# Kernel tuning notes

Measured on AMD Instinct MI355X. Metric: run time of the kernel, lower is better.

## Reference

```python
import jax, jax.numpy as jnp
import numpy as np

N = 20000       # nodes
E = 320000      # edges (before self-loops)
F_IN = 1024     # num_features
H = 4           # head_num
C = 64          # hidden_size
NC = 4          # n_classes
NEG_SLOPE = 0.2 # PyG GATConv default


def setup_inputs() -> dict:
    key = jax.random.key(0)
    ks = jax.random.split(key, 16)
    def w(k, shape, fan_in):
        return jax.random.normal(k, shape, dtype=jnp.float32) / np.sqrt(fan_in)
    x = jax.random.normal(ks[0], (N, F_IN), dtype=jnp.float32)
    edge_index = jax.random.randint(ks[1], (2, E), 0, N, dtype=jnp.int64)
    return {
        "x": x,
        "edge_index": edge_index,
        # layer 1: F_IN -> H*C, concat
        "w1": w(ks[2], (F_IN, H * C), F_IN),
        "as1": w(ks[3], (H, C), C),
        "ad1": w(ks[4], (H, C), C),
        "b1": jnp.zeros((H * C,), jnp.float32),
        # layer 2: H*C -> H*C, concat
        "w2": w(ks[5], (H * C, H * C), H * C),
        "as2": w(ks[6], (H, C), C),
        "ad2": w(ks[7], (H, C), C),
        "b2": jnp.zeros((H * C,), jnp.float32),
        # out layer: H*C -> C, 1 head, concat=False
        "w3": w(ks[8], (H * C, 1 * C), H * C),
        "as3": w(ks[9], (1, C), C),
        "ad3": w(ks[10], (1, C), C),
        "b3": jnp.zeros((C,), jnp.float32),
        # classifier
        "wc": w(ks[11], (C, NC), C),
        "bc": jnp.zeros((NC,), jnp.float32),
    }


def gat_layer(x, src, dst, W, a_src, a_dst, bias, concat):
    """PyG GATConv (eval mode, self-loops already added to src/dst)."""
    n = x.shape[0]
    Hh, Cc = a_src.shape
    h = (x @ W).reshape(n, Hh, Cc)                       # [N,H,C]
    al_s = jnp.sum(h * a_src[None], axis=-1)             # [N,H]
    al_d = jnp.sum(h * a_dst[None], axis=-1)             # [N,H]
    e = al_s[src] + al_d[dst]                            # [E,H]
    e = jax.nn.leaky_relu(e, NEG_SLOPE)
    # segment softmax over incoming edges of each destination node
    emax = jax.ops.segment_max(e, dst, num_segments=n)   # [N,H]
    ex = jnp.exp(e - emax[dst])
    denom = jax.ops.segment_sum(ex, dst, num_segments=n) # [N,H]
    alpha = ex / (denom[dst] + 1e-16)                    # [E,H]
    msg = h[src] * alpha[..., None]                      # [E,H,C]
    out = jax.ops.segment_sum(msg, dst, num_segments=n)  # [N,H,C]
    if concat:
        out = out.reshape(n, Hh * Cc)
    else:
        out = out.mean(axis=1)
    return out + bias


def reference(x, edge_index, w1, as1, ad1, b1, w2, as2, ad2, b2,
              w3, as3, ad3, b3, wc, bc):
    n = x.shape[0]
    loop = jnp.arange(n, dtype=edge_index.dtype)
    src = jnp.concatenate([edge_index[0], loop])
    dst = jnp.concatenate([edge_index[1], loop])
    out = jax.nn.relu(gat_layer(x, src, dst, w1, as1, ad1, b1, True))
    out = jax.nn.relu(gat_layer(out, src, dst, w2, as2, ad2, b2, True))
    out = gat_layer(out, src, dst, w3, as3, ad3, b3, False)
    return out @ wc + bc                                  # [N, n_classes]
```

## Files before the change

### kernel.cpp

```cpp
#include <hip/hip_runtime.h>

#define N_NODES 20000
#define N_EDGES 320000
#define ET (N_EDGES + N_NODES)
#define F_IN 1024
#define HC 256
#define NC 4

typedef unsigned short ushort_t;
typedef __attribute__((ext_vector_type(8))) short short8;
typedef __attribute__((ext_vector_type(4))) float f32x4;

__device__ inline ushort_t f2bf(float f) {
    unsigned u = __float_as_uint(f);
    unsigned r = (u + 0x7fffu + ((u >> 16) & 1u)) >> 16;
    return (ushort_t)r;
}
__device__ inline float bf2f(ushort_t u) {
    return __uint_as_float(((unsigned)u) << 16);
}

__device__ inline unsigned cvt_pk_bf16(float lo, float hi) {
    unsigned r;
    asm("v_cvt_pk_bf16_f32 %0, %1, %2" : "=v"(r) : "v"(lo), "v"(hi));
    return r;
}

#define GLOAD16(gp, lp) __builtin_amdgcn_global_load_lds( \
    (const __attribute__((address_space(1))) void*)(gp),  \
    (__attribute__((address_space(3))) void*)(lp), 16, 0, 0)

__global__ void count_kernel(const int* __restrict__ ei, int* __restrict__ counts) {
    int e = blockIdx.x * blockDim.x + threadIdx.x;
    if (e >= ET) return;
    int dst = (e < N_EDGES) ? ei[N_EDGES + e] : (e - N_EDGES);
    atomicAdd(&counts[dst], 1);
}

__global__ void scan_kernel(const int* __restrict__ counts, int* __restrict__ row_ptr,
                            int* __restrict__ cursor) {
    __shared__ int sums[1024];
    int t = threadIdx.x;
    const int per = (N_NODES + 1023) / 1024;
    int b = t * per;
    int e = min(b + per, N_NODES);
    int s = 0;
    for (int i = b; i < e; ++i) s += counts[i];
    sums[t] = s;
    __syncthreads();
    for (int off = 1; off < 1024; off <<= 1) {
        int v = (t >= off) ? sums[t - off] : 0;
        __syncthreads();
        sums[t] += v;
        __syncthreads();
    }
    int run = (t == 0) ? 0 : sums[t - 1];
    for (int i = b; i < e; ++i) {
        row_ptr[i] = run;
        cursor[i]  = run;
        run += counts[i];
    }
    if (t == 0) row_ptr[N_NODES] = ET;
}

__global__ void scatter_kernel(const int* __restrict__ ei, int* __restrict__ cursor,
                               int* __restrict__ col) {
    int e = blockIdx.x * blockDim.x + threadIdx.x;
    if (e >= ET) return;
    int src, dst;
    if (e < N_EDGES) { src = ei[e]; dst = ei[N_EDGES + e]; }
    else             { src = dst = e - N_EDGES; }
    int pos = atomicAdd(&cursor[dst], 1);
    col[pos] = src;
}

__global__ void split_T(const float* __restrict__ in, ushort_t* __restrict__ hi,
                        ushort_t* __restrict__ lo, int K, int Nn) {
    int idx = blockIdx.x * blockDim.x + threadIdx.x;
    if (idx >= K * Nn) return;
    int k = idx / Nn, n = idx - k * Nn;
    float v = in[idx];
    ushort_t h = f2bf(v);
    hi[(size_t)n * K + k] = h;
    lo[(size_t)n * K + k] = f2bf(v - bf2f(h));
}

#define AL_EPILOGUE()                                                              \
    {                                                                              \
        float asv[NF], adv[NF];                                                    \
        _Pragma("unroll")                                                          \
        for (int j = 0; j < NF; ++j) {                                             \
            int col = bn + wn * SN + j * 16 + (lane & 15);                         \
            asv[j] = as_w[col];                                                    \
            adv[j] = ad_w[col];                                                    \
        }                                                                          \
        float* s_as = (float*)smem;                                   \
        float* s_ad = (float*)smem + 2 * BM;                                       \
        _Pragma("unroll")                                                          \
        for (int i = 0; i < MF; ++i) {                                             \
            _Pragma("unroll")                                                      \
            for (int rr = 0; rr < 4; ++rr) {                                       \
                float ps = 0.f, pd = 0.f;                                          \
                _Pragma("unroll")                                                  \
                for (int j = 0; j < NF; ++j) {                                     \
                    ps += acc[i][j][rr] * asv[j];                                  \
                    pd += acc[i][j][rr] * adv[j];                                  \
                }                                                                  \
                _Pragma("unroll")                                                  \
                for (int o = 1; o < 16; o <<= 1) {                                 \
                    ps += __shfl_xor(ps, o, 64);                                   \
                    pd += __shfl_xor(pd, o, 64);                                   \
                }                                                                  \
                if ((lane & 15) == 0) {                                            \
                    int rl = wm * SM + i * 16 + (lane >> 4) * 4 + rr;              \
                    s_as[wn * BM + rl] = ps;                                       \
                    s_ad[wn * BM + rl] = pd;                                       \
                }                                                                  \
            }                                                                      \
        }                                                                          \
        __syncthreads();                                                           \
        if (t < BM) {                                                              \
            int row = bm + t;                                                      \
            if (row < M) {                                                         \
                int hb = bn >> 6;                                                  \
                als[row * H + hb] = s_as[t] + s_as[BM + t];                        \
                ald[row * H + hb] = s_ad[t] + s_ad[BM + t];                        \
            }                                                                      \
        }                                                                          \
    }

template<int GY>
__launch_bounds__(256)
__global__ void gemm_f32a_ks(const float* __restrict__ X,
                             const ushort_t* __restrict__ BTh, const ushort_t* __restrict__ BTl,
                             float* __restrict__ Cp0, float* __restrict__ Cp1,
                             int M, int K, int NT) {
    constexpr int BM = 128, BN = 64, SM = 64, SN = 32, MF = 4, NF = 2;
    __shared__ __align__(16) char smem[49152];

    const int t = threadIdx.x, lane = t & 63, w = t >> 6;
    const int wm = w >> 1, wn = w & 1;
    const int nwg = gridDim.x;
    const int id = blockIdx.x;
    const int q = nwg >> 3, r = nwg & 7;
    const int xcd = id & 7, idx = id >> 3;
    const int logical = (xcd < r ? xcd * (q + 1) : r * (q + 1) + (xcd - r) * q) + idx;
    const int nwg_half = nwg >> 1;
    const int ks = logical / nwg_half;
    const int rem = logical - ks * nwg_half;
    const int bm = (rem / GY) * BM, bn = (rem % GY) * BN;
    const int kbase = ks * (K >> 1);
    float* Cp = ks ? Cp1 : Cp0;

    const int achk = lane & 3;
    const float* xRow[2]; int aoff[2];
    #pragma unroll
    for (int qq = 0; qq < 2; ++qq) {
        int arow = (w * 2 + qq) * 16 + (lane >> 2);
        int grow = min(bm + arow, M - 1);
        xRow[qq] = X + (size_t)grow * K + kbase + achk * 8;
        aoff[qq] = arow * 64 + ((achk ^ ((arow >> 1) & 3)) * 16);
    }
    const int gchunk = ((lane & 3) ^ ((lane >> 3) & 3)) * 16;
    const int brow = w * 16 + (lane >> 2);
    const size_t gB = (size_t)(bn + brow) * K * 2 + (size_t)kbase * 2 + gchunk;
    const int lB = w * 1024;

    const char* Bhb = (const char*)BTh;
    const char* Blb = (const char*)BTl;
    const int c16 = (lane >> 4);
    const int NTs = K >> 7;

    f32x4 acc[MF][NF];
    #pragma unroll
    for (int i = 0; i < MF; ++i)
        #pragma unroll
        for (int j = 0; j < NF; ++j) acc[i][j] = (f32x4){0.f, 0.f, 0.f, 0.f};

    float4 cur0[2][2], cur1[2][2], nxt0[2][2], nxt1[2][2];
    #pragma unroll
    for (int qq = 0; qq < 2; ++qq)
        #pragma unroll
        for (int kc = 0; kc < 2; ++kc) {
            cur0[qq][kc] = *(const float4*)(xRow[qq] + kc * 32);
            cur1[qq][kc] = *(const float4*)(xRow[qq] + kc * 32 + 4);
        }

    for (int ts = 0; ts < NTs; ++ts) {
        size_t kb = (size_t)ts * 128;
        #pragma unroll
        for (int kc = 0; kc < 2; ++kc) {
            GLOAD16(Bhb + gB + kb + kc * 64, smem + 32768 + kc * 4096 + lB);
            GLOAD16(Blb + gB + kb + kc * 64, smem + 40960 + kc * 4096 + lB);
        }
        #pragma unroll
        for (int qq = 0; qq < 2; ++qq)
            #pragma unroll
            for (int kc = 0; kc < 2; ++kc) {
                float vv[8] = {cur0[qq][kc].x, cur0[qq][kc].y, cur0[qq][kc].z, cur0[qq][kc].w,
                               cur1[qq][kc].x, cur1[qq][kc].y, cur1[qq][kc].z, cur1[qq][kc].w};
                unsigned hp[4], lp[4];
                #pragma unroll
                for (int j = 0; j < 4; ++j) {
                    unsigned h = cvt_pk_bf16(vv[2 * j], vv[2 * j + 1]);
                    float h0 = __uint_as_float(h << 16);
                    float h1 = __uint_as_float(h & 0xFFFF0000u);
                    hp[j] = h;
                    lp[j] = cvt_pk_bf16(vv[2 * j] - h0, vv[2 * j + 1] - h1);
                }
                *(uint4*)(smem + kc * 8192 + aoff[qq])         = make_uint4(hp[0], hp[1], hp[2], hp[3]);
                *(uint4*)(smem + 16384 + kc * 8192 + aoff[qq]) = make_uint4(lp[0], lp[1], lp[2], lp[3]);
            }
        __syncthreads();
        if (ts + 1 < NTs) {
            int ko = (ts + 1) * 64;
            #pragma unroll
            for (int qq = 0; qq < 2; ++qq)
                #pragma unroll
                for (int kc = 0; kc < 2; ++kc) {
                    nxt0[qq][kc] = *(const float4*)(xRow[qq] + ko + kc * 32);
                    nxt1[qq][kc] = *(const float4*)(xRow[qq] + ko + kc * 32 + 4);
                }
        }
        #pragma unroll
        for (int kc = 0; kc < 2; ++kc) {
            short8 afh[MF], afl[MF], bfh[NF], bfl[NF];
            #pragma unroll
            for (int i = 0; i < MF; ++i) {
                int row = wm * SM + i * 16 + (lane & 15);
                int off = row * 64 + ((c16 ^ ((row >> 1) & 3)) * 16);
                afh[i] = *(const short8*)(smem + kc * 8192 + off);
                afl[i] = *(const short8*)(smem + 16384 + kc * 8192 + off);
            }
            #pragma unroll
            for (int j = 0; j < NF; ++j) {
                int row = wn * SN + j * 16 + (lane & 15);
                int off = row * 64 + ((c16 ^ ((row >> 1) & 3)) * 16);
                bfh[j] = *(const short8*)(smem + 32768 + kc * 4096 + off);
                bfl[j] = *(const short8*)(smem + 40960 + kc * 4096 + off);
            }
            #pragma unroll
            for (int i = 0; i < MF; ++i)
                #pragma unroll
                for (int j = 0; j < NF; ++j) {
                    acc[i][j] = __builtin_amdgcn_mfma_f32_16x16x32_bf16(afh[i], bfh[j], acc[i][j], 0, 0, 0);
                    acc[i][j] = __builtin_amdgcn_mfma_f32_16x16x32_bf16(afh[i], bfl[j], acc[i][j], 0, 0, 0);
                    acc[i][j] = __builtin_amdgcn_mfma_f32_16x16x32_bf16(afl[i], bfh[j], acc[i][j], 0, 0, 0);
                }
        }
        __syncthreads();
        #pragma unroll
        for (int qq = 0; qq < 2; ++qq)
            #pragma unroll
            for (int kc = 0; kc < 2; ++kc) { cur0[qq][kc] = nxt0[qq][kc]; cur1[qq][kc] = nxt1[qq][kc]; }
    }
    #pragma unroll
    for (int i = 0; i < MF; ++i) {
        int rbase = bm + wm * SM + i * 16 + (lane >> 4) * 4;
        #pragma unroll
        for (int j = 0; j < NF; ++j) {
            int col = bn + wn * SN + j * 16 + (lane & 15);
            #pragma unroll
            for (int rr = 0; rr < 4; ++rr)
                if (rbase + rr < M) Cp[(size_t)(rbase + rr) * NT + col] = acc[i][j][rr];
        }
    }
}

__launch_bounds__(256)
__global__ void reduce_al(float* __restrict__ B0, const float* __restrict__ Cp1,
                          const float* __restrict__ as_w, const float* __restrict__ ad_w,
                          float* __restrict__ als, float* __restrict__ ald) {
    int lane = threadIdx.x & 63, w = threadIdx.x >> 6;
    int row = blockIdx.x * 4 + w;
    if (row >= N_NODES) return;
    size_t base = (size_t)row * HC + lane * 4;
    float4 p0 = *(const float4*)&B0[base];
    float4 p1 = *(const float4*)&Cp1[base];
    float4 s = make_float4(p0.x + p1.x, p0.y + p1.y, p0.z + p1.z, p0.w + p1.w);
    *(float4*)&B0[base] = s;
    int head = lane >> 4;
    int cw = (lane & 15) * 4;
    float ps = s.x * as_w[head * 64 + cw + 0] + s.y * as_w[head * 64 + cw + 1]
             + s.z * as_w[head * 64 + cw + 2] + s.w * as_w[head * 64 + cw + 3];
    float pd = s.x * ad_w[head * 64 + cw + 0] + s.y * ad_w[head * 64 + cw + 1]
             + s.z * ad_w[head * 64 + cw + 2] + s.w * ad_w[head * 64 + cw + 3];
    #pragma unroll
    for (int o = 1; o < 16; o <<= 1) {
        ps += __shfl_xor(ps, o, 64);
        pd += __shfl_xor(pd, o, 64);
    }
    if ((lane & 15) == 0) {
        als[row * 4 + head] = ps;
        ald[row * 4 + head] = pd;
    }
}

template<int BMT, int GY, int H>
__launch_bounds__(256)
__global__ void gemm_mfma(const ushort_t* __restrict__ Ah, const ushort_t* __restrict__ Al,
                          const ushort_t* __restrict__ BTh, const ushort_t* __restrict__ BTl,
                          float* __restrict__ C, const float* __restrict__ as_w,
                          const float* __restrict__ ad_w, float* __restrict__ als,
                          float* __restrict__ ald, int M, int K, int NT) {
    constexpr int BM = BMT, BN = 64, SM = BM / 2, SN = 32, MF = SM / 16, NF = 2;
    constexpr int AQ = BM / 64;
    constexpr int ASZ = BM * 64;
    __shared__ __align__(16) char smem[4 * ASZ + 16384];

    const int t = threadIdx.x, lane = t & 63, w = t >> 6;
    const int wm = w >> 1, wn = w & 1;
    const int nwg = gridDim.x;
    const int id = blockIdx.x;
    const int q = nwg >> 3, r = nwg & 7;
    const int xcd = id & 7, idx = id >> 3;
    const int logical = (xcd < r ? xcd * (q + 1) : r * (q + 1) + (xcd - r) * q) + idx;
    const int bm = (logical / GY) * BM, bn = (logical % GY) * BN;
    const int gchunk = ((lane & 3) ^ ((lane >> 3) & 3)) * 16;

    size_t gA[AQ]; int lA[AQ];
    #pragma unroll
    for (int qq = 0; qq < AQ; ++qq) {
        int inst = w * AQ + qq;
        int arow = inst * 16 + (lane >> 2);
        int grow = min(bm + arow, M - 1);
        gA[qq] = (size_t)grow * K * 2 + gchunk;
        lA[qq] = inst * 1024;
    }
    const int brow = w * 16 + (lane >> 2);
    const size_t gB = (size_t)(bn + brow) * K * 2 + gchunk;
    const int lB = w * 1024;

    const char* Ahb = (const char*)Ah;
    const char* Alb = (const char*)Al;
    const char* Bhb = (const char*)BTh;
    const char* Blb = (const char*)BTl;
    const int c16 = (lane >> 4);
    const int NTs = K / 64;

    f32x4 acc[MF][NF];
    #pragma unroll
    for (int i = 0; i < MF; ++i)
        #pragma unroll
        for (int j = 0; j < NF; ++j) acc[i][j] = (f32x4){0.f, 0.f, 0.f, 0.f};

    for (int ts = 0; ts < NTs; ++ts) {
        size_t kb = (size_t)ts * 128;
        #pragma unroll
        for (int kc = 0; kc < 2; ++kc) {
            #pragma unroll
            for (int qq = 0; qq < AQ; ++qq) {
                GLOAD16(Ahb + gA[qq] + kb + kc * 64, smem + kc * ASZ + lA[qq]);
                GLOAD16(Alb + gA[qq] + kb + kc * 64, smem + 2 * ASZ + kc * ASZ + lA[qq]);
            }
            GLOAD16(Bhb + gB + kb + kc * 64, smem + 4 * ASZ + kc * 4096 + lB);
            GLOAD16(Blb + gB + kb + kc * 64, smem + 4 * ASZ + 8192 + kc * 4096 + lB);
        }
        __syncthreads();
        #pragma unroll
        for (int kc = 0; kc < 2; ++kc) {
            short8 afh[MF], afl[MF], bfh[NF], bfl[NF];
            #pragma unroll
            for (int i = 0; i < MF; ++i) {
                int row = wm * SM + i * 16 + (lane & 15);
                int off = row * 64 + ((c16 ^ ((row >> 1) & 3)) * 16);
                afh[i] = *(const short8*)(smem + kc * ASZ + off);
                afl[i] = *(const short8*)(smem + 2 * ASZ + kc * ASZ + off);
            }
            #pragma unroll
            for (int j = 0; j < NF; ++j) {
                int row = wn * SN + j * 16 + (lane & 15);
                int off = row * 64 + ((c16 ^ ((row >> 1) & 3)) * 16);
                bfh[j] = *(const short8*)(smem + 4 * ASZ + kc * 4096 + off);
                bfl[j] = *(const short8*)(smem + 4 * ASZ + 8192 + kc * 4096 + off);
            }
            #pragma unroll
            for (int i = 0; i < MF; ++i)
                #pragma unroll
                for (int j = 0; j < NF; ++j) {
                    acc[i][j] = __builtin_amdgcn_mfma_f32_16x16x32_bf16(afh[i], bfh[j], acc[i][j], 0, 0, 0);
                    acc[i][j] = __builtin_amdgcn_mfma_f32_16x16x32_bf16(afh[i], bfl[j], acc[i][j], 0, 0, 0);
                    acc[i][j] = __builtin_amdgcn_mfma_f32_16x16x32_bf16(afl[i], bfh[j], acc[i][j], 0, 0, 0);
                }
        }
        __syncthreads();
    }
    #pragma unroll
    for (int i = 0; i < MF; ++i) {
        int rbase = bm + wm * SM + i * 16 + (lane >> 4) * 4;
        #pragma unroll
        for (int j = 0; j < NF; ++j) {
            int col = bn + wn * SN + j * 16 + (lane & 15);
            #pragma unroll
            for (int rr = 0; rr < 4; ++rr)
                if (rbase + rr < M) C[(size_t)(rbase + rr) * NT + col] = acc[i][j][rr];
        }
    }
    AL_EPILOGUE()
}

template<int H>
__launch_bounds__(256)
__global__ void alpha_kernel(const float* __restrict__ als, const float* __restrict__ ald,
                             const int* __restrict__ row_ptr, const int* __restrict__ col,
                             float* __restrict__ alpha) {
    int lane = threadIdx.x & 63, w = threadIdx.x >> 6;
    int dst = blockIdx.x * 4 + w;
    if (dst >= N_NODES) return;
    int beg = row_ptr[dst], deg = row_ptr[dst + 1] - beg;
    constexpr int ES = 64 / H;
    int i_loc = lane / H, hh = lane % H;
    float ad = ald[dst * H + hh];
    float m = -1e30f, den = 0.f;
    for (int base = 0; base < deg; base += ES) {
        int i = base + i_loc;
        if (i < deg) {
            float e = als[col[beg + i] * H + hh] + ad;
            e = (e > 0.f) ? e : 0.2f * e;
            float nm = fmaxf(m, e);
            den = den * __expf(m - nm) + __expf(e - nm);
            m = nm;
        }
    }
    #pragma unroll
    for (int off = H; off < 64; off <<= 1) {
        float mo = __shfl_xor(m, off, 64);
        float dn = __shfl_xor(den, off, 64);
        float nm = fmaxf(m, mo);
        den = den * __expf(m - nm) + dn * __expf(mo - nm);
        m = nm;
    }
    float rden = 1.f / (den + 1e-16f);
    for (int base = 0; base < deg; base += ES) {
        int i = base + i_loc;
        if (i < deg) {
            float e = als[col[beg + i] * H + hh] + ad;
            e = (e > 0.f) ? e : 0.2f * e;
            alpha[(size_t)hh * ET + beg + i] = __expf(e - m) * rden;
        }
    }
}

template<int CT, int CW, int H, bool RELU, bool SPLIT, bool CLS>
__launch_bounds__(256)
__global__ void agg_v5(const float* __restrict__ h, const float* __restrict__ alpha,
                       const int* __restrict__ row_ptr, const int* __restrict__ col,
                       const float* __restrict__ bias,
                       ushort_t* __restrict__ oh, ushort_t* __restrict__ ol,
                       float* __restrict__ of,
                       const float* __restrict__ wc, const float* __restrict__ bc,
                       float* __restrict__ cls_out) {
    constexpr int NS  = CT / CW;
    constexpr int LPT = CW / 4;
    constexpr int TPW = 64 / LPT;
    static_assert(NS == H, "slice==head mapping");
    __shared__ int   s_src[4][64];
    __shared__ float s_alp[4][64];
    const int nwg = gridDim.x;
    const int q = nwg >> 3;
    int id = blockIdx.x;
    int logical = (id & 7) * q + (id >> 3);
    int slice = logical / (N_NODES / 4);
    int g = logical - slice * (N_NODES / 4);
    int lane = threadIdx.x & 63, w = threadIdx.x >> 6;
    int dst = g * 4 + w;
    int beg = row_ptr[dst], deg = row_ptr[dst + 1] - beg;
    int team = lane / LPT;
    int cc = (lane & (LPT - 1)) * 4;

    const int*   colP = col + beg;
    const float* aP   = alpha + (size_t)slice * ET + beg;
    const float* hS   = h + slice * CW + cc;

    float4 a0v = make_float4(0.f, 0.f, 0.f, 0.f);
    float4 a1v = make_float4(0.f, 0.f, 0.f, 0.f);
    float4 a2v = make_float4(0.f, 0.f, 0.f, 0.f);
    float4 a3v = make_float4(0.f, 0.f, 0.f, 0.f);
    for (int base = 0; base < deg; base += 64) {
        int cnt = min(64, deg - base);
        if (lane < cnt) {
            s_src[w][lane] = colP[base + lane];
            s_alp[w][lane] = aP[base + lane];
        }
        int i = team;
        for (; i + 3 * TPW < cnt; i += 4 * TPW) {
            int   s0 = s_src[w][i],           s1 = s_src[w][i + TPW];
            int   s2 = s_src[w][i + 2 * TPW], s3 = s_src[w][i + 3 * TPW];
            float a0 = s_alp[w][i],           a1 = s_alp[w][i + TPW];
            float a2 = s_alp[w][i + 2 * TPW], a3 = s_alp[w][i + 3 * TPW];
            float4 h0 = *(const float4*)&hS[s0 * CT];
            float4 h1 = *(const float4*)&hS[s1 * CT];
            float4 h2 = *(const float4*)&hS[s2 * CT];
            float4 h3 = *(const float4*)&hS[s3 * CT];
            a0v.x += a0 * h0.x; a0v.y += a0 * h0.y; a0v.z += a0 * h0.z; a0v.w += a0 * h0.w;
            a1v.x += a1 * h1.x; a1v.y += a1 * h1.y; a1v.z += a1 * h1.z; a1v.w += a1 * h1.w;
            a2v.x += a2 * h2.x; a2v.y += a2 * h2.y; a2v.z += a2 * h2.z; a2v.w += a2 * h2.w;
            a3v.x += a3 * h3.x; a3v.y += a3 * h3.y; a3v.z += a3 * h3.z; a3v.w += a3 * h3.w;
        }
        for (; i < cnt; i += TPW) {
            int   s0 = s_src[w][i];
            float a0 = s_alp[w][i];
            float4 h0 = *(const float4*)&hS[s0 * CT];
            a0v.x += a0 * h0.x; a0v.y += a0 * h0.y; a0v.z += a0 * h0.z; a0v.w += a0 * h0.w;
        }
    }
    float4 acc = make_float4((a0v.x + a1v.x) + (a2v.x + a3v.x),
                             (a0v.y + a1v.y) + (a2v.y + a3v.y),
                             (a0v.z + a1v.z) + (a2v.z + a3v.z),
                             (a0v.w + a1v.w) + (a2v.w + a3v.w));
    #pragma unroll
    for (int off = LPT; off < 64; off <<= 1) {
        acc.x += __shfl_xor(acc.x, off, 64);
        acc.y += __shfl_xor(acc.y, off, 64);
        acc.z += __shfl_xor(acc.z, off, 64);
        acc.w += __shfl_xor(acc.w, off, 64);
    }
    if (team == 0) {
        int ch = slice * CW + cc;
        float4 bv = *(const float4*)&bias[ch];
        float v0 = acc.x + bv.x, v1 = acc.y + bv.y, v2 = acc.z + bv.z, v3 = acc.w + bv.w;
        if (RELU) {
            v0 = fmaxf(v0, 0.f); v1 = fmaxf(v1, 0.f);
            v2 = fmaxf(v2, 0.f); v3 = fmaxf(v3, 0.f);
        }
        if (CLS) {
            float ps[NC];
            #pragma unroll
            for (int k = 0; k < NC; ++k)
                ps[k] = v0 * wc[(cc + 0) * NC + k] + v1 * wc[(cc + 1) * NC + k]
                      + v2 * wc[(cc + 2) * NC + k] + v3 * wc[(cc + 3) * NC + k];
            #pragma unroll
            for (int o = 1; o < 16; o <<= 1)
                #pragma unroll
                for (int k = 0; k < NC; ++k) ps[k] += __shfl_xor(ps[k], o, 64);
            if (lane == 0) {
                #pragma unroll
                for (int k = 0; k < NC; ++k) cls_out[(size_t)dst * NC + k] = ps[k] + bc[k];
            }
        } else {
            size_t idx = (size_t)dst * CT + ch;
            if (SPLIT) {
                ushort4 h4, l4;
                h4.x = f2bf(v0); l4.x = f2bf(v0 - bf2f(h4.x));
                h4.y = f2bf(v1); l4.y = f2bf(v1 - bf2f(h4.y));
                h4.z = f2bf(v2); l4.z = f2bf(v2 - bf2f(h4.z));
                h4.w = f2bf(v3); l4.w = f2bf(v3 - bf2f(h4.w));
                *(ushort4*)&oh[idx] = h4;
                *(ushort4*)&ol[idx] = l4;
            } else {
                *(float4*)&of[idx] = make_float4(v0, v1, v2, v3);
            }
        }
    }
}

extern "C" void kernel_launch(void* const* d_in, const int* in_sizes, int n_in,
                              void* d_out, int out_size, void* d_ws, size_t ws_size,
                              hipStream_t stream) {
    const float* x   = (const float*)d_in[0];
    const int*   ei  = (const int*)d_in[1];
    const float* w1  = (const float*)d_in[2];
    const float* as1 = (const float*)d_in[3];
    const float* ad1 = (const float*)d_in[4];
    const float* b1  = (const float*)d_in[5];
    const float* w2  = (const float*)d_in[6];
    const float* as2 = (const float*)d_in[7];
    const float* ad2 = (const float*)d_in[8];
    const float* b2  = (const float*)d_in[9];
    const float* w3  = (const float*)d_in[10];
    const float* as3 = (const float*)d_in[11];
    const float* ad3 = (const float*)d_in[12];
    const float* b3  = (const float*)d_in[13];
    const float* wc  = (const float*)d_in[14];
    const float* bc  = (const float*)d_in[15];
    float* out = (float*)d_out;

    char* ws = (char*)d_ws;
    size_t off = 0;
    auto alloc = [&](size_t bytes) -> char* {
        char* p = ws + off;
        off = (off + bytes + 255) & ~(size_t)255;
        return p;
    };

    int* counts  = (int*)alloc(N_NODES * 4);
    int* cursor  = (int*)alloc(N_NODES * 4);
    int* row_ptr = (int*)alloc((N_NODES + 1) * 4);
    int* colidx  = (int*)alloc(ET * 4);
    float* als   = (float*)alloc(N_NODES * 4 * 4);
    float* ald   = (float*)alloc(N_NODES * 4 * 4);
    float* alpha = (float*)alloc((size_t)4 * ET * 4);
    float* B0    = (float*)alloc((size_t)N_NODES * HC * 4);
    float* Cp1   = (float*)alloc((size_t)N_NODES * HC * 4);

    ushort_t* w1Th = (ushort_t*)alloc((size_t)F_IN * HC * 2);
    ushort_t* w1Tl = (ushort_t*)alloc((size_t)F_IN * HC * 2);
    ushort_t* w2Th = (ushort_t*)alloc((size_t)HC * HC * 2);
    ushort_t* w2Tl = (ushort_t*)alloc((size_t)HC * HC * 2);
    ushort_t* w3Th = (ushort_t*)alloc((size_t)HC * 64 * 2);
    ushort_t* w3Tl = (ushort_t*)alloc((size_t)HC * 64 * 2);
    ushort_t* B1h  = (ushort_t*)alloc((size_t)N_NODES * HC * 2);
    ushort_t* B1l  = (ushort_t*)alloc((size_t)N_NODES * HC * 2);

    hipMemsetAsync(counts, 0, N_NODES * sizeof(int), stream);
    int eb = (ET + 255) / 256;
    count_kernel<<<eb, 256, 0, stream>>>(ei, counts);
    scan_kernel<<<1, 1024, 0, stream>>>(counts, row_ptr, cursor);
    scatter_kernel<<<eb, 256, 0, stream>>>(ei, cursor, colidx);

    split_T<<<(F_IN * HC + 255) / 256, 256, 0, stream>>>(w1, w1Th, w1Tl, F_IN, HC);
    split_T<<<(HC * HC + 255) / 256, 256, 0, stream>>>(w2, w2Th, w2Tl, HC, HC);
    split_T<<<(HC * 64 + 255) / 256, 256, 0, stream>>>(w3, w3Th, w3Tl, HC, 64);

    const int nwg128 = ((N_NODES + 127) / 128) * (HC / 64);
    const int nblk_dst = N_NODES / 4;
    gemm_f32a_ks<4><<<2 * nwg128, 256, 0, stream>>>(x, w1Th, w1Tl, B0, Cp1, N_NODES, F_IN, HC);
    reduce_al<<<nblk_dst, 256, 0, stream>>>(B0, Cp1, as1, ad1, als, ald);
    alpha_kernel<4><<<nblk_dst, 256, 0, stream>>>(als, ald, row_ptr, colidx, alpha);
    agg_v5<256, 64, 4, true, true, false><<<4 * nblk_dst, 256, 0, stream>>>(
        B0, alpha, row_ptr, colidx, b1, B1h, B1l, nullptr, nullptr, nullptr, nullptr);
    gemm_mfma<128, 4, 4><<<nwg128, 256, 0, stream>>>(B1h, B1l, w2Th, w2Tl, B0, as2, ad2,
                                                     als, ald, N_NODES, HC, HC);
    alpha_kernel<4><<<nblk_dst, 256, 0, stream>>>(als, ald, row_ptr, colidx, alpha);
    agg_v5<256, 64, 4, true, true, false><<<4 * nblk_dst, 256, 0, stream>>>(
        B0, alpha, row_ptr, colidx, b2, B1h, B1l, nullptr, nullptr, nullptr, nullptr);
    const int nwg3 = (N_NODES + 63) / 64;
    gemm_mfma<64, 1, 1><<<nwg3, 256, 0, stream>>>(B1h, B1l, w3Th, w3Tl, B0, as3, ad3,
                                                  als, ald, N_NODES, HC, 64);
    alpha_kernel<1><<<nblk_dst, 256, 0, stream>>>(als, ald, row_ptr, colidx, alpha);
    agg_v5<64, 64, 1, false, false, true><<<nblk_dst, 256, 0, stream>>>(
        B0, alpha, row_ptr, colidx, b3, nullptr, nullptr, nullptr, wc, bc, out);
}
```

Before: 283.9 us.

## Fuse edge softmax into aggregation and halve GEMM K-tile to cut LDS

The separate alpha_kernel pass is removed. Each aggregation warp now computes an online max/denominator over its destination's incoming edges and recomputes the normalized attention weights while staging source indices, so the per-edge alpha array is neither written nor read back. In the layer-1 split-K GEMM, the K step per iteration drops from 128 to 64, which halves shared memory (49152 to 24576 bytes) and the prefetch registers, likely to raise occupancy. The trade-offs are redundant softmax and exp work on each head-slice warp in aggregation, and twice as many GEMM iterations and barriers.

```diff
diff --git a/kernel.cpp b/kernel.cpp
--- a/kernel.cpp
+++ b/kernel.cpp
@@ -136,7 +136,7 @@
                              float* __restrict__ Cp0, float* __restrict__ Cp1,
                              int M, int K, int NT) {
     constexpr int BM = 128, BN = 64, SM = 64, SN = 32, MF = 4, NF = 2;
-    __shared__ __align__(16) char smem[49152];
+    __shared__ __align__(16) char smem[24576];
 
     const int t = threadIdx.x, lane = t & 63, w = t >> 6;
     const int wm = w >> 1, wn = w & 1;
@@ -169,7 +169,7 @@
     const char* Bhb = (const char*)BTh;
     const char* Blb = (const char*)BTl;
     const int c16 = (lane >> 4);
-    const int NTs = K >> 7;
+    const int NTs = K >> 6;
 
     f32x4 acc[MF][NF];
     #pragma unroll
@@ -177,82 +177,68 @@
         #pragma unroll
         for (int j = 0; j < NF; ++j) acc[i][j] = (f32x4){0.f, 0.f, 0.f, 0.f};
 
-    float4 cur0[2][2], cur1[2][2], nxt0[2][2], nxt1[2][2];
-    #pragma unroll
-    for (int qq = 0; qq < 2; ++qq)
-        #pragma unroll
-        for (int kc = 0; kc < 2; ++kc) {
-            cur0[qq][kc] = *(const float4*)(xRow[qq] + kc * 32);
-            cur1[qq][kc] = *(const float4*)(xRow[qq] + kc * 32 + 4);
-        }
+    float4 cur0[2], cur1[2], nxt0[2], nxt1[2];
+    #pragma unroll
+    for (int qq = 0; qq < 2; ++qq) {
+        cur0[qq] = *(const float4*)(xRow[qq]);
+        cur1[qq] = *(const float4*)(xRow[qq] + 4);
+    }
 
     for (int ts = 0; ts < NTs; ++ts) {
-        size_t kb = (size_t)ts * 128;
-        #pragma unroll
-        for (int kc = 0; kc < 2; ++kc) {
-            GLOAD16(Bhb + gB + kb + kc * 64, smem + 32768 + kc * 4096 + lB);
-            GLOAD16(Blb + gB + kb + kc * 64, smem + 40960 + kc * 4096 + lB);
-        }
-        #pragma unroll
-        for (int qq = 0; qq < 2; ++qq)
-            #pragma unroll
-            for (int kc = 0; kc < 2; ++kc) {
-                float vv[8] = {cur0[qq][kc].x, cur0[qq][kc].y, cur0[qq][kc].z, cur0[qq][kc].w,
-                               cur1[qq][kc].x, cur1[qq][kc].y, cur1[qq][kc].z, cur1[qq][kc].w};
-                unsigned hp[4], lp[4];
-                #pragma unroll
-                for (int j = 0; j < 4; ++j) {
-                    unsigned h = cvt_pk_bf16(vv[2 * j], vv[2 * j + 1]);
-                    float h0 = __uint_as_float(h << 16);
-                    float h1 = __uint_as_float(h & 0xFFFF0000u);
-                    hp[j] = h;
-                    lp[j] = cvt_pk_bf16(vv[2 * j] - h0, vv[2 * j + 1] - h1);
-                }
-                *(uint4*)(smem + kc * 8192 + aoff[qq])         = make_uint4(hp[0], hp[1], hp[2], hp[3]);
-                *(uint4*)(smem + 16384 + kc * 8192 + aoff[qq]) = make_uint4(lp[0], lp[1], lp[2], lp[3]);
-            }
+        size_t kb = (size_t)ts * 64;
+        GLOAD16(Bhb + gB + kb, smem + 16384 + lB);
+        GLOAD16(Blb + gB + kb, smem + 20480 + lB);
+        #pragma unroll
+        for (int qq = 0; qq < 2; ++qq) {
+            float vv[8] = {cur0[qq].x, cur0[qq].y, cur0[qq].z, cur0[qq].w,
+                           cur1[qq].x, cur1[qq].y, cur1[qq].z, cur1[qq].w};
+            unsigned hp[4], lp[4];
+            #pragma unroll
+            for (int j = 0; j < 4; ++j) {
+                unsigned h = cvt_pk_bf16(vv[2 * j], vv[2 * j + 1]);
+                float h0 = __uint_as_float(h << 16);
+                float h1 = __uint_as_float(h & 0xFFFF0000u);
+                hp[j] = h;
+                lp[j] = cvt_pk_bf16(vv[2 * j] - h0, vv[2 * j + 1] - h1);
+            }
+            *(uint4*)(smem + aoff[qq])        = make_uint4(hp[0], hp[1], hp[2], hp[3]);
+            *(uint4*)(smem + 8192 + aoff[qq]) = make_uint4(lp[0], lp[1], lp[2], lp[3]);
+        }
         __syncthreads();
         if (ts + 1 < NTs) {
-            int ko = (ts + 1) * 64;
-            #pragma unroll
-            for (int qq = 0; qq < 2; ++qq)
-                #pragma unroll
-                for (int kc = 0; kc < 2; ++kc) {
-                    nxt0[qq][kc] = *(const float4*)(xRow[qq] + ko + kc * 32);
-                    nxt1[qq][kc] = *(const float4*)(xRow[qq] + ko + kc * 32 + 4);
-                }
-        }
-        #pragma unroll
-        for (int kc = 0; kc < 2; ++kc) {
-            short8 afh[MF], afl[MF], bfh[NF], bfl[NF];
-            #pragma unroll
-            for (int i = 0; i < MF; ++i) {
-                int row = wm * SM + i * 16 + (lane & 15);
-                int off = row * 64 + ((c16 ^ ((row >> 1) & 3)) * 16);
-                afh[i] = *(const short8*)(smem + kc * 8192 + off);
-                afl[i] = *(const short8*)(smem + 16384 + kc * 8192 + off);
-            }
+            int ko = (ts + 1) * 32;
+            #pragma unroll
+            for (int qq = 0; qq < 2; ++qq) {
+                nxt0[qq] = *(const float4*)(xRow[qq] + ko);
+                nxt1[qq] = *(const float4*)(xRow[qq] + ko + 4);
+            }
+        }
+        short8 afh[MF], afl[MF], bfh[NF], bfl[NF];
+        #pragma unroll
+        for (int i = 0; i < MF; ++i) {
+            int row = wm * SM + i * 16 + (lane & 15);
+            int off = row * 64 + ((c16 ^ ((row >> 1) & 3)) * 16);
+            afh[i] = *(const short8*)(smem + off);
+            afl[i] = *(const short8*)(smem + 8192 + off);
+        }
+        #pragma unroll
+        for (int j = 0; j < NF; ++j) {
+            int row = wn * SN + j * 16 + (lane & 15);
+            int off = row * 64 + ((c16 ^ ((row >> 1) & 3)) * 16);
+            bfh[j] = *(const short8*)(smem + 16384 + off);
+            bfl[j] = *(const short8*)(smem + 20480 + off);
+        }
+        #pragma unroll
+        for (int i = 0; i < MF; ++i)
             #pragma unroll
             for (int j = 0; j < NF; ++j) {
-                int row = wn * SN + j * 16 + (lane & 15);
-                int off = row * 64 + ((c16 ^ ((row >> 1) & 3)) * 16);
-                bfh[j] = *(const short8*)(smem + 32768 + kc * 4096 + off);
-                bfl[j] = *(const short8*)(smem + 40960 + kc * 4096 + off);
-            }
-            #pragma unroll
-            for (int i = 0; i < MF; ++i)
-                #pragma unroll
-                for (int j = 0; j < NF; ++j) {
-                    acc[i][j] = __builtin_amdgcn_mfma_f32_16x16x32_bf16(afh[i], bfh[j], acc[i][j], 0, 0, 0);
-                    acc[i][j] = __builtin_amdgcn_mfma_f32_16x16x32_bf16(afh[i], bfl[j], acc[i][j], 0, 0, 0);
-                    acc[i][j] = __builtin_amdgcn_mfma_f32_16x16x32_bf16(afl[i], bfh[j], acc[i][j], 0, 0, 0);
-                }
-        }
+                acc[i][j] = __builtin_amdgcn_mfma_f32_16x16x32_bf16(afh[i], bfh[j], acc[i][j], 0, 0, 0);
+                acc[i][j] = __builtin_amdgcn_mfma_f32_16x16x32_bf16(afh[i], bfl[j], acc[i][j], 0, 0, 0);
+                acc[i][j] = __builtin_amdgcn_mfma_f32_16x16x32_bf16(afl[i], bfh[j], acc[i][j], 0, 0, 0);
+            }
         __syncthreads();
         #pragma unroll
-        for (int qq = 0; qq < 2; ++qq)
-            #pragma unroll
-            for (int kc = 0; kc < 2; ++kc) { cur0[qq][kc] = nxt0[qq][kc]; cur1[qq][kc] = nxt1[qq][kc]; }
+        for (int qq = 0; qq < 2; ++qq) { cur0[qq] = nxt0[qq]; cur1[qq] = nxt1[qq]; }
     }
     #pragma unroll
     for (int i = 0; i < MF; ++i) {
@@ -399,51 +385,10 @@
     AL_EPILOGUE()
 }
 
-template<int H>
-__launch_bounds__(256)
-__global__ void alpha_kernel(const float* __restrict__ als, const float* __restrict__ ald,
-                             const int* __restrict__ row_ptr, const int* __restrict__ col,
-                             float* __restrict__ alpha) {
-    int lane = threadIdx.x & 63, w = threadIdx.x >> 6;
-    int dst = blockIdx.x * 4 + w;
-    if (dst >= N_NODES) return;
-    int beg = row_ptr[dst], deg = row_ptr[dst + 1] - beg;
-    constexpr int ES = 64 / H;
-    int i_loc = lane / H, hh = lane % H;
-    float ad = ald[dst * H + hh];
-    float m = -1e30f, den = 0.f;
-    for (int base = 0; base < deg; base += ES) {
-        int i = base + i_loc;
-        if (i < deg) {
-            float e = als[col[beg + i] * H + hh] + ad;
-            e = (e > 0.f) ? e : 0.2f * e;
-            float nm = fmaxf(m, e);
-            den = den * __expf(m - nm) + __expf(e - nm);
-            m = nm;
-        }
-    }
-    #pragma unroll
-    for (int off = H; off < 64; off <<= 1) {
-        float mo = __shfl_xor(m, off, 64);
-        float dn = __shfl_xor(den, off, 64);
-        float nm = fmaxf(m, mo);
-        den = den * __expf(m - nm) + dn * __expf(mo - nm);
-        m = nm;
-    }
-    float rden = 1.f / (den + 1e-16f);
-    for (int base = 0; base < deg; base += ES) {
-        int i = base + i_loc;
-        if (i < deg) {
-            float e = als[col[beg + i] * H + hh] + ad;
-            e = (e > 0.f) ? e : 0.2f * e;
-            alpha[(size_t)hh * ET + beg + i] = __expf(e - m) * rden;
-        }
-    }
-}
-
 template<int CT, int CW, int H, bool RELU, bool SPLIT, bool CLS>
 __launch_bounds__(256)
-__global__ void agg_v5(const float* __restrict__ h, const float* __restrict__ alpha,
+__global__ void agg_v6(const float* __restrict__ h, const float* __restrict__ als,
+                       const float* __restrict__ ald,
                        const int* __restrict__ row_ptr, const int* __restrict__ col,
                        const float* __restrict__ bias,
                        ushort_t* __restrict__ oh, ushort_t* __restrict__ ol,
@@ -469,8 +414,29 @@
     int cc = (lane & (LPT - 1)) * 4;
 
     const int*   colP = col + beg;
-    const float* aP   = alpha + (size_t)slice * ET + beg;
     const float* hS   = h + slice * CW + cc;
+    float ad = ald[dst * H + slice];
+
+    float m = -1e30f, den = 0.f;
+    for (int base = 0; base < deg; base += 64) {
+        int i = base + lane;
+        if (i < deg) {
+            float e = als[colP[i] * H + slice] + ad;
+            e = (e > 0.f) ? e : 0.2f * e;
+            float nm = fmaxf(m, e);
+            den = den * __expf(m - nm) + __expf(e - nm);
+            m = nm;
+        }
+    }
+    #pragma unroll
+    for (int off = 1; off < 64; off <<= 1) {
+        float mo = __shfl_xor(m, off, 64);
+        float dn = __shfl_xor(den, off, 64);
+        float nm = fmaxf(m, mo);
+        den = den * __expf(m - nm) + dn * __expf(mo - nm);
+        m = nm;
+    }
+    float rden = 1.f / (den + 1e-16f);
 
     float4 a0v = make_float4(0.f, 0.f, 0.f, 0.f);
     float4 a1v = make_float4(0.f, 0.f, 0.f, 0.f);
@@ -479,8 +445,11 @@
     for (int base = 0; base < deg; base += 64) {
         int cnt = min(64, deg - base);
         if (lane < cnt) {
-            s_src[w][lane] = colP[base + lane];
-            s_alp[w][lane] = aP[base + lane];
+            int src = colP[base + lane];
+            s_src[w][lane] = src;
+            float e = als[src * H + slice] + ad;
+            e = (e > 0.f) ? e : 0.2f * e;
+            s_alp[w][lane] = __expf(e - m) * rden;
         }
         int i = team;
         for (; i + 3 * TPW < cnt; i += 4 * TPW) {
@@ -589,7 +558,6 @@
     int* colidx  = (int*)alloc(ET * 4);
     float* als   = (float*)alloc(N_NODES * 4 * 4);
     float* ald   = (float*)alloc(N_NODES * 4 * 4);
-    float* alpha = (float*)alloc((size_t)4 * ET * 4);
     float* B0    = (float*)alloc((size_t)N_NODES * HC * 4);
     float* Cp1   = (float*)alloc((size_t)N_NODES * HC * 4);
 
@@ -616,18 +584,15 @@
     const int nblk_dst = N_NODES / 4;
     gemm_f32a_ks<4><<<2 * nwg128, 256, 0, stream>>>(x, w1Th, w1Tl, B0, Cp1, N_NODES, F_IN, HC);
     reduce_al<<<nblk_dst, 256, 0, stream>>>(B0, Cp1, as1, ad1, als, ald);
-    alpha_kernel<4><<<nblk_dst, 256, 0, stream>>>(als, ald, row_ptr, colidx, alpha);
-    agg_v5<256, 64, 4, true, true, false><<<4 * nblk_dst, 256, 0, stream>>>(
-        B0, alpha, row_ptr, colidx, b1, B1h, B1l, nullptr, nullptr, nullptr, nullptr);
+    agg_v6<256, 64, 4, true, true, false><<<4 * nblk_dst, 256, 0, stream>>>(
+        B0, als, ald, row_ptr, colidx, b1, B1h, B1l, nullptr, nullptr, nullptr, nullptr);
     gemm_mfma<128, 4, 4><<<nwg128, 256, 0, stream>>>(B1h, B1l, w2Th, w2Tl, B0, as2, ad2,
                                                      als, ald, N_NODES, HC, HC);
-    alpha_kernel<4><<<nblk_dst, 256, 0, stream>>>(als, ald, row_ptr, colidx, alpha);
-    agg_v5<256, 64, 4, true, true, false><<<4 * nblk_dst, 256, 0, stream>>>(
-        B0, alpha, row_ptr, colidx, b2, B1h, B1l, nullptr, nullptr, nullptr, nullptr);
+    agg_v6<256, 64, 4, true, true, false><<<4 * nblk_dst, 256, 0, stream>>>(
+        B0, als, ald, row_ptr, colidx, b2, B1h, B1l, nullptr, nullptr, nullptr, nullptr);
     const int nwg3 = (N_NODES + 63) / 64;
     gemm_mfma<64, 1, 1><<<nwg3, 256, 0, stream>>>(B1h, B1l, w3Th, w3Tl, B0, as3, ad3,
                                                   als, ald, N_NODES, HC, 64);
-    alpha_kernel<1><<<nblk_dst, 256, 0, stream>>>(als, ald, row_ptr, colidx, alpha);
-    agg_v5<64, 64, 1, false, false, true><<<nblk_dst, 256, 0, stream>>>(
-        B0, alpha, row_ptr, colidx, b3, nullptr, nullptr, nullptr, wc, bc, out);
-}
+    agg_v6<64, 64, 1, false, false, true><<<nblk_dst, 256, 0, stream>>>(
+        B0, als, ald, row_ptr, colidx, b3, nullptr, nullptr, nullptr, wc, bc, out);
+}
```

New measurement: 288.8 us. No clear change (+1.7%).

## Fuse edge-softmax alpha computation into aggregation kernel

Applied to the files above, without the earlier changes.

Removes the separate alpha_kernel launches and the 4*ET alpha buffer. Each aggregation wavefront now computes the online softmax max and denominator for its destination and head slice, then recomputes normalized alpha while staging source indices into shared memory. This saves three kernel launches plus the alpha write and read traffic. In exchange the als gathers and exp work are repeated inside the aggregation, and with one head per slice the softmax pass now uses 64 edges per lane group instead of 16.

```diff
diff --git a/kernel.cpp b/kernel.cpp
--- a/kernel.cpp
+++ b/kernel.cpp
@@ -399,51 +399,10 @@
     AL_EPILOGUE()
 }
 
-template<int H>
-__launch_bounds__(256)
-__global__ void alpha_kernel(const float* __restrict__ als, const float* __restrict__ ald,
-                             const int* __restrict__ row_ptr, const int* __restrict__ col,
-                             float* __restrict__ alpha) {
-    int lane = threadIdx.x & 63, w = threadIdx.x >> 6;
-    int dst = blockIdx.x * 4 + w;
-    if (dst >= N_NODES) return;
-    int beg = row_ptr[dst], deg = row_ptr[dst + 1] - beg;
-    constexpr int ES = 64 / H;
-    int i_loc = lane / H, hh = lane % H;
-    float ad = ald[dst * H + hh];
-    float m = -1e30f, den = 0.f;
-    for (int base = 0; base < deg; base += ES) {
-        int i = base + i_loc;
-        if (i < deg) {
-            float e = als[col[beg + i] * H + hh] + ad;
-            e = (e > 0.f) ? e : 0.2f * e;
-            float nm = fmaxf(m, e);
-            den = den * __expf(m - nm) + __expf(e - nm);
-            m = nm;
-        }
-    }
-    #pragma unroll
-    for (int off = H; off < 64; off <<= 1) {
-        float mo = __shfl_xor(m, off, 64);
-        float dn = __shfl_xor(den, off, 64);
-        float nm = fmaxf(m, mo);
-        den = den * __expf(m - nm) + dn * __expf(mo - nm);
-        m = nm;
-    }
-    float rden = 1.f / (den + 1e-16f);
-    for (int base = 0; base < deg; base += ES) {
-        int i = base + i_loc;
-        if (i < deg) {
-            float e = als[col[beg + i] * H + hh] + ad;
-            e = (e > 0.f) ? e : 0.2f * e;
-            alpha[(size_t)hh * ET + beg + i] = __expf(e - m) * rden;
-        }
-    }
-}
-
 template<int CT, int CW, int H, bool RELU, bool SPLIT, bool CLS>
 __launch_bounds__(256)
-__global__ void agg_v5(const float* __restrict__ h, const float* __restrict__ alpha,
+__global__ void agg_v6(const float* __restrict__ h, const float* __restrict__ als,
+                       const float* __restrict__ ald,
                        const int* __restrict__ row_ptr, const int* __restrict__ col,
                        const float* __restrict__ bias,
                        ushort_t* __restrict__ oh, ushort_t* __restrict__ ol,
@@ -469,8 +428,29 @@
     int cc = (lane & (LPT - 1)) * 4;
 
     const int*   colP = col + beg;
-    const float* aP   = alpha + (size_t)slice * ET + beg;
     const float* hS   = h + slice * CW + cc;
+    float ad = ald[dst * H + slice];
+
+    float m = -1e30f, den = 0.f;
+    for (int base = 0; base < deg; base += 64) {
+        int i = base + lane;
+        if (i < deg) {
+            float e = als[colP[i] * H + slice] + ad;
+            e = (e > 0.f) ? e : 0.2f * e;
+            float nm = fmaxf(m, e);
+            den = den * __expf(m - nm) + __expf(e - nm);
+            m = nm;
+        }
+    }
+    #pragma unroll
+    for (int off = 1; off < 64; off <<= 1) {
+        float mo = __shfl_xor(m, off, 64);
+        float dn = __shfl_xor(den, off, 64);
+        float nm = fmaxf(m, mo);
+        den = den * __expf(m - nm) + dn * __expf(mo - nm);
+        m = nm;
+    }
+    float rden = 1.f / (den + 1e-16f);
 
     float4 a0v = make_float4(0.f, 0.f, 0.f, 0.f);
     float4 a1v = make_float4(0.f, 0.f, 0.f, 0.f);
@@ -479,8 +459,11 @@
     for (int base = 0; base < deg; base += 64) {
         int cnt = min(64, deg - base);
         if (lane < cnt) {
-            s_src[w][lane] = colP[base + lane];
-            s_alp[w][lane] = aP[base + lane];
+            int src = colP[base + lane];
+            s_src[w][lane] = src;
+            float e = als[src * H + slice] + ad;
+            e = (e > 0.f) ? e : 0.2f * e;
+            s_alp[w][lane] = __expf(e - m) * rden;
         }
         int i = team;
         for (; i + 3 * TPW < cnt; i += 4 * TPW) {
@@ -589,7 +572,6 @@
     int* colidx  = (int*)alloc(ET * 4);
     float* als   = (float*)alloc(N_NODES * 4 * 4);
     float* ald   = (float*)alloc(N_NODES * 4 * 4);
-    float* alpha = (float*)alloc((size_t)4 * ET * 4);
     float* B0    = (float*)alloc((size_t)N_NODES * HC * 4);
     float* Cp1   = (float*)alloc((size_t)N_NODES * HC * 4);
 
@@ -616,18 +598,15 @@
     const int nblk_dst = N_NODES / 4;
     gemm_f32a_ks<4><<<2 * nwg128, 256, 0, stream>>>(x, w1Th, w1Tl, B0, Cp1, N_NODES, F_IN, HC);
     reduce_al<<<nblk_dst, 256, 0, stream>>>(B0, Cp1, as1, ad1, als, ald);
-    alpha_kernel<4><<<nblk_dst, 256, 0, stream>>>(als, ald, row_ptr, colidx, alpha);
-    agg_v5<256, 64, 4, true, true, false><<<4 * nblk_dst, 256, 0, stream>>>(
-        B0, alpha, row_ptr, colidx, b1, B1h, B1l, nullptr, nullptr, nullptr, nullptr);
+    agg_v6<256, 64, 4, true, true, false><<<4 * nblk_dst, 256, 0, stream>>>(
+        B0, als, ald, row_ptr, colidx, b1, B1h, B1l, nullptr, nullptr, nullptr, nullptr);
     gemm_mfma<128, 4, 4><<<nwg128, 256, 0, stream>>>(B1h, B1l, w2Th, w2Tl, B0, as2, ad2,
                                                      als, ald, N_NODES, HC, HC);
-    alpha_kernel<4><<<nblk_dst, 256, 0, stream>>>(als, ald, row_ptr, colidx, alpha);
-    agg_v5<256, 64, 4, true, true, false><<<4 * nblk_dst, 256, 0, stream>>>(
-        B0, alpha, row_ptr, colidx, b2, B1h, B1l, nullptr, nullptr, nullptr, nullptr);
+    agg_v6<256, 64, 4, true, true, false><<<4 * nblk_dst, 256, 0, stream>>>(
+        B0, als, ald, row_ptr, colidx, b2, B1h, B1l, nullptr, nullptr, nullptr, nullptr);
     const int nwg3 = (N_NODES + 63) / 64;
     gemm_mfma<64, 1, 1><<<nwg3, 256, 0, stream>>>(B1h, B1l, w3Th, w3Tl, B0, as3, ad3,
                                                   als, ald, N_NODES, HC, 64);
-    alpha_kernel<1><<<nblk_dst, 256, 0, stream>>>(als, ald, row_ptr, colidx, alpha);
-    agg_v5<64, 64, 1, false, false, true><<<nblk_dst, 256, 0, stream>>>(
-        B0, alpha, row_ptr, colidx, b3, nullptr, nullptr, nullptr, wc, bc, out);
-}
+    agg_v6<64, 64, 1, false, false, true><<<nblk_dst, 256, 0, stream>>>(
+        B0, als, ald, row_ptr, colidx, b3, nullptr, nullptr, nullptr, wc, bc, out);
+}
```

Result: no change. 285.2 us (+0.4%).
